# Optimization experiments

Hardware: AMD Instinct MI355X
Metric: run time of the kernel (lower is better)

The kernel has to match this reference:

```python
import jax, jax.numpy as jnp
import numpy as np
from jax import lax

EPS = 1e-5

def _bn(x, g, b, m, v):
    # eval-mode BatchNorm2d over channel dim of NCHW
    return (x - m[None, :, None, None]) * (g / jnp.sqrt(v + EPS))[None, :, None, None] + b[None, :, None, None]


def _forward(x, proj_w, proj_b, bn0_g, bn0_b, bn0_m, bn0_v,
             in_proj_w, conv_w, conv_b, x_proj_w, dt_w, dt_b, A_log, D,
             out_proj_w, fc_w, fc_b,
             c1_w, c1_b, bn1_g, bn1_b, bn1_m, bn1_v,
             c2_w, c2_b, bn2_g, bn2_b, bn2_m, bn2_v):
    d_state = A_log.shape[1]
    # ---- spectral projection: 1x1 conv + BN + ReLU ----
    p = jnp.einsum('bchw,dc->bdhw', x, proj_w) + proj_b[None, :, None, None]
    p = jax.nn.relu(_bn(p, bn0_g, bn0_b, bn0_m, bn0_v))
    b, d, h, w = p.shape
    L = h * w
    tok = p.reshape(b, d, L).transpose(0, 2, 1)            # [b, L, d_model]

    # ---- Mamba block (d_model=32, d_state=16, d_conv=4, expand=2) ----
    xz = tok @ in_proj_w.T                                 # [b, L, 2*d_in]
    d_in = xz.shape[-1] // 2
    xm, z = xz[..., :d_in], xz[..., d_in:]
    # causal depthwise conv1d along sequence
    xc = lax.conv_general_dilated(
        xm.transpose(0, 2, 1), conv_w[:, None, :], (1,),
        [(conv_w.shape[-1] - 1, 0)], feature_group_count=d_in,
        dimension_numbers=('NCH', 'OIH', 'NCH'))
    u = jax.nn.silu(xc + conv_b[None, :, None]).transpose(0, 2, 1)  # [b, L, d_in]
    xdbl = u @ x_proj_w.T                                  # [b, L, dt_rank+2N]
    dt_rank = dt_w.shape[1]
    dt = xdbl[..., :dt_rank]
    Bm = xdbl[..., dt_rank:dt_rank + d_state]              # [b, L, N]
    Cm = xdbl[..., dt_rank + d_state:]                     # [b, L, N]
    delta = jax.nn.softplus(dt @ dt_w.T + dt_b)            # [b, L, d_in]
    A = -jnp.exp(A_log)                                    # [d_in, N]

    def step(hst, inp):
        d_t, B_t, C_t, u_t = inp                           # [b,d_in],[b,N],[b,N],[b,d_in]
        dA = jnp.exp(d_t[..., None] * A)                   # [b, d_in, N]
        hst = dA * hst + (d_t * u_t)[..., None] * B_t[:, None, :]
        y_t = jnp.einsum('bdn,bn->bd', hst, C_t)
        return hst, y_t

    h0 = jnp.zeros((b, d_in, d_state), dtype=u.dtype)
    xs = (delta.transpose(1, 0, 2), Bm.transpose(1, 0, 2),
          Cm.transpose(1, 0, 2), u.transpose(1, 0, 2))
    _, ys = lax.scan(step, h0, xs)                         # [L, b, d_in]
    y = ys.transpose(1, 0, 2) + u * D                      # D skip
    y = y * jax.nn.silu(z)                                 # gated
    m_out = y @ out_proj_w.T                               # [b, L, d_model]
    mamba_feat = (m_out @ fc_w.T + fc_b).mean(axis=1)      # [b, FEATURE_DIM]

    # ---- CNN branch ----
    dn = ('NCHW', 'OIHW', 'NCHW')
    c = lax.conv_general_dilated(p, c1_w, (1, 1), 'VALID', dimension_numbers=dn) + c1_b[None, :, None, None]
    c = jax.nn.relu(_bn(c, bn1_g, bn1_b, bn1_m, bn1_v))
    c = lax.conv_general_dilated(c, c2_w, (1, 1), 'VALID', dimension_numbers=dn) + c2_b[None, :, None, None]
    c = jax.nn.relu(_bn(c, bn2_g, bn2_b, bn2_m, bn2_v))
    cnn_feat = c.mean(axis=(2, 3))                         # AdaptiveAvgPool2d(1)+Flatten
    return mamba_feat + cnn_feat


def setup_inputs() -> dict:
    key = jax.random.key(0)
    ks = jax.random.split(key, 16)
    B, C_IN, P = 128, 200, 32
    D_MODEL, D_IN, N, DTR, FDIM = 32, 64, 16, 2, 128
    r = lambda k, s, sc=0.05: jax.random.normal(k, s, jnp.float32) * sc
    f32 = jnp.float32
    return {
        'x': jax.random.normal(ks[0], (B, C_IN, P, P), f32),
        'proj_w': r(ks[1], (D_MODEL, C_IN)),
        'proj_b': jnp.zeros((D_MODEL,), f32),
        'bn0_g': jnp.ones((D_MODEL,), f32), 'bn0_b': jnp.zeros((D_MODEL,), f32),
        'bn0_m': jnp.zeros((D_MODEL,), f32), 'bn0_v': jnp.ones((D_MODEL,), f32),
        'in_proj_w': r(ks[2], (2 * D_IN, D_MODEL)),
        'conv_w': r(ks[3], (D_IN, 4), 0.3),
        'conv_b': jnp.zeros((D_IN,), f32),
        'x_proj_w': r(ks[4], (DTR + 2 * N, D_IN)),
        'dt_w': r(ks[5], (D_IN, DTR), 0.5),
        'dt_b': r(ks[6], (D_IN,), 0.5) - 4.0,
        'A_log': jnp.tile(jnp.log(jnp.arange(1, N + 1, dtype=f32))[None, :], (D_IN, 1)),
        'D': jnp.ones((D_IN,), f32),
        'out_proj_w': r(ks[7], (D_MODEL, D_IN)),
        'fc_w': r(ks[8], (FDIM, D_MODEL)),
        'fc_b': jnp.zeros((FDIM,), f32),
        'c1_w': r(ks[9], (32, D_MODEL, 3, 3)),
        'c1_b': jnp.zeros((32,), f32),
        'bn1_g': jnp.ones((32,), f32), 'bn1_b': jnp.zeros((32,), f32),
        'bn1_m': jnp.zeros((32,), f32), 'bn1_v': jnp.ones((32,), f32),
        'c2_w': r(ks[10], (FDIM, 32, 3, 3)),
        'c2_b': jnp.zeros((FDIM,), f32),
        'bn2_g': jnp.ones((FDIM,), f32), 'bn2_b': jnp.zeros((FDIM,), f32),
        'bn2_m': jnp.zeros((FDIM,), f32), 'bn2_v': jnp.ones((FDIM,), f32),
    }


def reference(x, proj_w, proj_b, bn0_g, bn0_b, bn0_m, bn0_v,
              in_proj_w, conv_w, conv_b, x_proj_w, dt_w, dt_b, A_log, D,
              out_proj_w, fc_w, fc_b,
              c1_w, c1_b, bn1_g, bn1_b, bn1_m, bn1_v,
              c2_w, c2_b, bn2_g, bn2_b, bn2_m, bn2_v):
    return _forward(x, proj_w, proj_b, bn0_g, bn0_b, bn0_m, bn0_v,
                    in_proj_w, conv_w, conv_b, x_proj_w, dt_w, dt_b, A_log, D,
                    out_proj_w, fc_w, fc_b,
                    c1_w, c1_b, bn1_g, bn1_b, bn1_m, bn1_v,
                    c2_w, c2_b, bn2_g, bn2_b, bn2_m, bn2_v)
```

## Files before the change

kernel.cpp:

```cpp
#include <hip/hip_runtime.h>
#include <cstdint>

typedef short bf16x8 __attribute__((ext_vector_type(8)));
typedef float f32x4 __attribute__((ext_vector_type(4)));
#define MFMA16(a, b, c) __builtin_amdgcn_mfma_f32_16x16x32_bf16((a), (b), (c), 0, 0, 0)

static __device__ __forceinline__ float fastrcp(float x) {
  float r;
  asm("v_rcp_f32 %0, %1" : "=v"(r) : "v"(x));
  return r;
}
static __device__ __forceinline__ float fastexp2(float x) {
  float r;
  asm("v_exp_f32 %0, %1" : "=v"(r) : "v"(x));
  return r;
}
static __device__ __forceinline__ float silu_(float x) {
  return x * fastrcp(1.f + __expf(-x));
}
static __device__ __forceinline__ unsigned short f2bf(float f) {
  union { float f; unsigned u; } v; v.f = f;
  unsigned r = v.u + 0x7FFF + ((v.u >> 16) & 1);
  return (unsigned short)(r >> 16);
}
static __device__ __forceinline__ void bf2x(unsigned p, float& lo, float& hi) {
  union { unsigned u; float f; } a, bb;
  a.u = p << 16; bb.u = p & 0xffff0000u;
  lo = a.f; hi = bb.f;
}
static __device__ __forceinline__ float bflo(unsigned short h) {
  union { unsigned u; float f; } a;
  a.u = ((unsigned)h) << 16;
  return a.f;
}

__global__ __launch_bounds__(256) void k_prep(
    const float* __restrict__ c1_w, const float* __restrict__ c2_w,
    const float* __restrict__ fc_w, const float* __restrict__ opw,
    const float* __restrict__ in_w, const float* __restrict__ xp_w,
    const float* __restrict__ pw,
    unsigned short* __restrict__ Wf1, unsigned short* __restrict__ Wf2,
    unsigned short* __restrict__ Wfin, unsigned short* __restrict__ Wfxp,
    unsigned short* __restrict__ Wfp,
    float* __restrict__ W2, float* __restrict__ cnn_sum)
{
  int i = blockIdx.x * 256 + threadIdx.x;
  if (i < 36864) {
    int j = i & 7, l = (i >> 3) & 63, m = (i >> 9) & 7, t = i >> 12;
    int co = m * 16 + (l & 15), ci = ((l >> 4) << 3) + j;
    Wf2[i] = f2bf(c2_w[(size_t)(co * 32 + ci) * 9 + t]);
  } else if (i < 46080) {
    int ii = i - 36864;
    int j = ii & 7, l = (ii >> 3) & 63, m = (ii >> 9) & 1, t = ii >> 10;
    int co = m * 16 + (l & 15), ci = ((l >> 4) << 3) + j;
    Wf1[ii] = f2bf(c1_w[(size_t)(co * 32 + ci) * 9 + t]);
  } else if (i < 54272) {
    int ii = i - 46080;
    int f = ii >> 6, d2 = ii & 63;
    float a = 0.f;
    #pragma unroll
    for (int dm = 0; dm < 32; dm++) a = fmaf(fc_w[(f << 5) + dm], opw[(dm << 6) + d2], a);
    W2[ii] = a;
  } else if (i < 70656) {
    cnn_sum[i - 54272] = 0.f;
  } else if (i < 74752) {
    int ii = i - 70656;
    int j = ii & 7, l = (ii >> 3) & 63, ot = ii >> 9;
    int o = (ot << 4) + (l & 15), c = ((l >> 4) << 3) + j;
    Wfin[ii] = f2bf(in_w[(o << 5) + c]);
  } else if (i < 77824) {
    int ii = i - 74752;
    int j = ii & 7, l = (ii >> 3) & 63, kh = (ii >> 9) & 1, ot = ii >> 10;
    int jr = (ot << 4) + (l & 15), c = (kh << 5) + ((l >> 4) << 3) + j;
    Wfxp[ii] = (jr < 34) ? f2bf(xp_w[(jr << 6) + c]) : (unsigned short)0;
  } else if (i < 84992) {
    int ii = i - 77824;
    int j = ii & 7, l = (ii >> 3) & 63, m = (ii >> 9) & 1, kt = ii >> 10;
    int co = (m << 4) + (l & 15), c = (kt << 5) + ((l >> 4) << 3) + j;
    Wfp[ii] = (c < 200) ? f2bf(pw[co * 200 + c]) : (unsigned short)0;
  }
}

__global__ __launch_bounds__(256, 4) void k_proj_m(
    const float* __restrict__ x, const unsigned short* __restrict__ Wfp,
    const float* __restrict__ pb,
    const float* __restrict__ g, const float* __restrict__ be,
    const float* __restrict__ mm, const float* __restrict__ vv,
    unsigned short* __restrict__ p_bf)
{
  __shared__ __align__(16) unsigned xT[2][256 * 20];
  int b = blockIdx.x >> 2, l0 = (blockIdx.x & 3) << 8;
  int tid = threadIdx.x, lane = tid & 63, w = tid >> 6;
  int li = lane & 15, kg4 = (lane >> 4) << 2;
  float scv[2][4], sbv[2][4];
  #pragma unroll
  for (int m = 0; m < 2; m++)
    #pragma unroll
    for (int jj = 0; jj < 4; jj++) {
      int co = m * 16 + ((lane >> 4) << 2) + jj;
      float s = g[co] * rsqrtf(vv[co] + 1e-5f);
      scv[m][jj] = s;
      sbv[m][jj] = fmaf(pb[co] - mm[co], s, be[co]);
    }
  const float* xb = x + (size_t)b * 200 * 1024 + l0 + tid;
  #pragma unroll
  for (int p = 0; p < 16; p++) {
    float v0 = xb[(2 * p) << 10];
    float v1 = xb[(2 * p + 1) << 10];
    xT[0][tid * 20 + p] = (unsigned)f2bf(v0) | ((unsigned)f2bf(v1) << 16);
  }
  __syncthreads();
  f32x4 acc[4][2];
  #pragma unroll
  for (int q = 0; q < 4; q++) {
    acc[q][0] = (f32x4){0.f, 0.f, 0.f, 0.f};
    acc[q][1] = (f32x4){0.f, 0.f, 0.f, 0.f};
  }
  int buf = 0;
  for (int kt = 0; kt < 7; kt++) {
    if (kt < 6) {
      const float* xc = xb + (((size_t)(kt + 1)) << 15);
      int cb = (kt + 1) * 32;
      #pragma unroll
      for (int p = 0; p < 16; p++) {
        int c = cb + 2 * p;
        float v0 = (c < 200) ? xc[(2 * p) << 10] : 0.f;
        float v1 = (c + 1 < 200) ? xc[(2 * p + 1) << 10] : 0.f;
        xT[buf ^ 1][tid * 20 + p] = (unsigned)f2bf(v0) | ((unsigned)f2bf(v1) << 16);
      }
    }
    bf16x8 a0 = *reinterpret_cast<const bf16x8*>(&Wfp[(((kt << 1) + 0) * 64 + lane) << 3]);
    bf16x8 a1 = *reinterpret_cast<const bf16x8*>(&Wfp[(((kt << 1) + 1) * 64 + lane) << 3]);
    #pragma unroll
    for (int q = 0; q < 4; q++) {
      int px = ((w + (q << 2)) << 4) + li;
      bf16x8 bfr = *reinterpret_cast<const bf16x8*>(&xT[buf][px * 20 + kg4]);
      acc[q][0] = MFMA16(a0, bfr, acc[q][0]);
      acc[q][1] = MFMA16(a1, bfr, acc[q][1]);
    }
    __syncthreads();
    buf ^= 1;
  }
  #pragma unroll
  for (int q = 0; q < 4; q++) {
    int px = ((w + (q << 2)) << 4) + li;
    size_t obase = (((size_t)b << 10) + l0 + px) << 5;
    #pragma unroll
    for (int m = 0; m < 2; m++) {
      f32x4 av = acc[q][m];
      ushort4 pk;
      pk.x = f2bf(fmaxf(fmaf(av[0], scv[m][0], sbv[m][0]), 0.f));
      pk.y = f2bf(fmaxf(fmaf(av[1], scv[m][1], sbv[m][1]), 0.f));
      pk.z = f2bf(fmaxf(fmaf(av[2], scv[m][2], sbv[m][2]), 0.f));
      pk.w = f2bf(fmaxf(fmaf(av[3], scv[m][3], sbv[m][3]), 0.f));
      *reinterpret_cast<ushort4*>(&p_bf[obase + m * 16 + ((lane >> 4) << 2)]) = pk;
    }
  }
}

__global__ __launch_bounds__(1024, 4) void k_mamba(
    const unsigned short* __restrict__ p_bf,
    const unsigned short* __restrict__ Wfin,
    const unsigned short* __restrict__ Wfxp,
    const float* __restrict__ conv_w,
    const float* __restrict__ conv_b,
    const float* __restrict__ dt_w,
    const float* __restrict__ dt_b,
    const float* __restrict__ A_log,
    float* __restrict__ pqrs,
    float* __restrict__ au_g)
{
  __shared__ __align__(16) char smem[65072];
  float* xm  = (float*)smem;
  float* dlS = (float*)smem;
  unsigned short* ubS  = (unsigned short*)(smem + 18224);
  unsigned short* uTb  = (unsigned short*)(smem + 27440);
  unsigned short* duzP = (unsigned short*)(smem + 36656);
  float* bcT  = (float*)(smem + 54064);
  float* cwS  = (float*)(smem + 62768);
  float* cbS  = (float*)(smem + 63792);
  float* dtwS = (float*)(smem + 64048);
  float* dtbS = (float*)(smem + 64560);
  float* auS  = (float*)(smem + 64816);

  int b = blockIdx.x >> 4, ch = blockIdx.x & 15;
  int tid = threadIdx.x, lane = tid & 63, w = tid >> 6;
  int li = lane & 15, cig8 = (lane >> 4) << 3;

  if (tid < 256) cwS[tid] = conv_w[tid];
  else if (tid < 320) cbS[tid - 256] = conv_b[tid - 256];
  else if (tid < 448) dtwS[tid - 320] = dt_w[tid - 320];
  else if (tid < 512) dtbS[tid - 448] = dt_b[tid - 448];
  else if (tid < 576) auS[tid - 512] = 0.f;

  const unsigned short* pbf_b = p_bf + ((size_t)b << 15);

  for (int j = w; j < 36; j += 16) {
    if (j < 20) {
      int ot = j / 5, tt = j % 5;
      int r = tt * 16 + li;
      int tg = (ch << 6) + r - 3;
      bf16x8 bfr = {0,0,0,0,0,0,0,0};
      if (r < 67 && tg >= 0)
        bfr = *reinterpret_cast<const bf16x8*>(pbf_b + ((size_t)tg << 5) + cig8);
      bf16x8 aW = *reinterpret_cast<const bf16x8*>(&Wfin[((ot << 6) + lane) << 3]);
      f32x4 acc = {0.f, 0.f, 0.f, 0.f};
      acc = MFMA16(aW, bfr, acc);
      if (r < 67)
        *reinterpret_cast<float4*>(&xm[r * 68 + (ot << 4) + ((lane >> 4) << 2)]) =
            make_float4(acc[0], acc[1], acc[2], acc[3]);
    } else {
      int jz = j - 20;
      int zot = jz >> 2, tt = jz & 3;
      int t = tt * 16 + li;
      int tg = (ch << 6) + t;
      bf16x8 bfr = *reinterpret_cast<const bf16x8*>(pbf_b + ((size_t)tg << 5) + cig8);
      bf16x8 aW = *reinterpret_cast<const bf16x8*>(&Wfin[(((4 + zot) << 6) + lane) << 3]);
      f32x4 acc = {0.f, 0.f, 0.f, 0.f};
      acc = MFMA16(aW, bfr, acc);
      int dzb = (zot << 4) + ((lane >> 4) << 2);
      int toff = ((t >> 2) << 3) + 4 + (t & 3);
      #pragma unroll
      for (int q = 0; q < 4; q++)
        duzP[(dzb + q) * 136 + toff] = f2bf(silu_(acc[q]));
    }
  }
  __syncthreads();
  {
    int d2 = tid & 63, oct = tid >> 6;
    int t0 = oct << 2;
    float4 cw4 = *reinterpret_cast<const float4*>(&cwS[d2 << 2]);
    float cb1 = cbS[d2];
    float x0 = xm[t0 * 68 + d2], x1 = xm[(t0 + 1) * 68 + d2], x2 = xm[(t0 + 2) * 68 + d2];
    uint2 zz2 = *reinterpret_cast<const uint2*>(&duzP[d2 * 136 + (oct << 3) + 4]);
    float zf[4];
    bf2x(zz2.x, zf[0], zf[1]); bf2x(zz2.y, zf[2], zf[3]);
    unsigned short up[4];
    float aup = 0.f;
    #pragma unroll
    for (int s = 0; s < 4; s++) {
      int t = t0 + s;
      float x3 = xm[(t + 3) * 68 + d2];
      float a = cb1;
      a = fmaf(cw4.x, x0, a); a = fmaf(cw4.y, x1, a);
      a = fmaf(cw4.z, x2, a); a = fmaf(cw4.w, x3, a);
      float uu = silu_(a);
      unsigned short ub_ = f2bf(uu);
      ubS[t * 72 + d2] = ub_;
      up[s] = ub_;
      aup = fmaf(uu, zf[s], aup);
      x0 = x1; x1 = x2; x2 = x3;
    }
    uint2 pk;
    pk.x = (unsigned)up[0] | ((unsigned)up[1] << 16);
    pk.y = (unsigned)up[2] | ((unsigned)up[3] << 16);
    *reinterpret_cast<uint2*>(&uTb[d2 * 72 + t0]) = pk;
    atomicAdd(&auS[d2], aup);
  }
  __syncthreads();
  if (w < 12) {
    int ot = w >> 2, tt = w & 3;
    int t = tt * 16 + li;
    const unsigned short* ub = &ubS[t * 72];
    bf16x8 b0 = *reinterpret_cast<const bf16x8*>(ub + cig8);
    bf16x8 b1 = *reinterpret_cast<const bf16x8*>(ub + 32 + cig8);
    bf16x8 a0 = *reinterpret_cast<const bf16x8*>(&Wfxp[(((ot << 1) + 0) * 64 + lane) << 3]);
    bf16x8 a1 = *reinterpret_cast<const bf16x8*>(&Wfxp[(((ot << 1) + 1) * 64 + lane) << 3]);
    f32x4 acc = {0.f, 0.f, 0.f, 0.f};
    acc = MFMA16(a0, b0, acc);
    acc = MFMA16(a1, b1, acc);
    int jb = (ot << 4) + ((lane >> 4) << 2);
    #pragma unroll
    for (int q = 0; q < 4; q++) {
      int jj = jb + q;
      if (jj < 2) bcT[(t & 31) * 68 + 64 + (jj << 1) + (t >> 5)] = acc[q];
      else if (jj < 34) bcT[(jj - 2) * 68 + t] = acc[q];
    }
  }
  __syncthreads();
  {
    int t = tid >> 4, dq = (tid & 15) << 2;
    int tr = t & 31, th = t >> 5;
    float d0 = bcT[tr * 68 + 64 + th];
    float d1 = bcT[tr * 68 + 66 + th];
    int toff = ((t >> 2) << 3) + (t & 3);
    #pragma unroll
    for (int q = 0; q < 4; q++) {
      int dg = dq + q;
      float pre = fmaf(d0, dtwS[dg << 1], fmaf(d1, dtwS[(dg << 1) + 1], dtbS[dg]));
      float dl_ = (pre > 20.f) ? pre : __logf(1.f + __expf(pre));
      dlS[dg * 68 + t] = dl_;
      float uf = bflo(uTb[dg * 72 + t]);
      duzP[dg * 136 + toff] = f2bf(dl_ * uf);
    }
  }
  __syncthreads();
  {
    int sd = tid >> 4, sn = tid & 15;
    float Areg2 = -__expf(A_log[(sd << 4) + sn]) * 1.44269504f;
    float P = 1.f, qq = 0.f, R = 0.f, S = 0.f;
    const float* dr = &dlS[sd * 68];
    const unsigned short* dz = &duzP[sd * 136];
    const float* Br = &bcT[sn * 68];
    const float* Cr = &bcT[(16 + sn) * 68];
    for (int g = 0; g < 16; g++) {
      float4 dv = *reinterpret_cast<const float4*>(dr + (g << 2));
      uint4 duz = *reinterpret_cast<const uint4*>(dz + (g << 3));
      float4 Bv = *reinterpret_cast<const float4*>(Br + (g << 2));
      float4 Cv = *reinterpret_cast<const float4*>(Cr + (g << 2));
      float du0, du1, du2, du3, z0, z1, z2, z3;
      bf2x(duz.x, du0, du1); bf2x(duz.y, du2, du3);
      bf2x(duz.z, z0, z1);  bf2x(duz.w, z2, z3);
      float e0 = fastexp2(dv.x * Areg2), e1 = fastexp2(dv.y * Areg2);
      float e2 = fastexp2(dv.z * Areg2), e3 = fastexp2(dv.w * Areg2);
      float c0 = Cv.x * z0, c1 = Cv.y * z1, c2 = Cv.z * z2, c3 = Cv.w * z3;
      P = e0 * P; qq = fmaf(e0, qq, du0 * Bv.x); R = fmaf(c0, P, R); S = fmaf(c0, qq, S);
      P = e1 * P; qq = fmaf(e1, qq, du1 * Bv.y); R = fmaf(c1, P, R); S = fmaf(c1, qq, S);
      P = e2 * P; qq = fmaf(e2, qq, du2 * Bv.z); R = fmaf(c2, P, R); S = fmaf(c2, qq, S);
      P = e3 * P; qq = fmaf(e3, qq, du3 * Bv.w); R = fmaf(c3, P, R); S = fmaf(c3, qq, S);
    }
    size_t idx = ((((size_t)b << 4) + ch) << 10) + (sd << 4) + sn;
    *reinterpret_cast<float4*>(pqrs + (idx << 2)) = make_float4(P, qq, R, S);
    if (sn == 0) au_g[((((size_t)b << 4) + ch) << 6) + sd] = auS[sd];
  }
}

__global__ __launch_bounds__(512) void k_comb(
    const float* __restrict__ pqrs, const float* __restrict__ au_g,
    const float* __restrict__ Dp, float* __restrict__ ybar)
{
  int b = blockIdx.x >> 1, hh = blockIdx.x & 1;
  int tid = threadIdx.x;
  int sd = (hh << 5) + (tid >> 4), sn = tid & 15;
  float4 pq[16];
  #pragma unroll
  for (int c = 0; c < 16; c++) {
    size_t idx = ((((size_t)b << 4) + c) << 10) + (sd << 4) + sn;
    pq[c] = *reinterpret_cast<const float4*>(pqrs + (idx << 2));
  }
  float h = 0.f, y = 0.f;
  #pragma unroll
  for (int c = 0; c < 16; c++) {
    y = fmaf(pq[c].z, h, y + pq[c].w);
    h = fmaf(pq[c].x, h, pq[c].y);
  }
  float val = y + Dp[sd] * au_g[((((size_t)b << 4) + sn) << 6) + sd];
  val += __shfl_xor(val, 1); val += __shfl_xor(val, 2);
  val += __shfl_xor(val, 4); val += __shfl_xor(val, 8);
  if (sn == 0) ybar[(b << 6) + sd] = val * (1.f / 1024.f);
}

__global__ __launch_bounds__(256) void k_conv1m(
    const unsigned short* __restrict__ p_bf, const unsigned short* __restrict__ Wf1,
    const float* __restrict__ cbias,
    const float* __restrict__ g, const float* __restrict__ be,
    const float* __restrict__ mm, const float* __restrict__ vv,
    unsigned short* __restrict__ c1_bf)
{
  __shared__ __align__(16) unsigned short inS[8 * 32 * 40];
  int b = blockIdx.x / 5, s = blockIdx.x % 5;
  int y0 = s * 6;
  int tid = threadIdx.x, lane = tid & 63, w = tid >> 6;
  int li = lane & 15, cig8 = (lane >> 4) << 3;
  for (int uu = tid; uu < 1024; uu += 256) {
    int r = uu >> 7, rem = uu & 127;
    uint4 v = *reinterpret_cast<const uint4*>(
        &p_bf[((((size_t)b << 10) + (y0 + r) * 32) << 5) + rem * 8]);
    int xx = rem >> 2, cg = rem & 3;
    *reinterpret_cast<uint4*>(&inS[(r * 32 + xx) * 40 + cg * 8]) = v;
  }
  bf16x8 aw[9][2];
  #pragma unroll
  for (int t = 0; t < 9; t++)
    #pragma unroll
    for (int m = 0; m < 2; m++)
      aw[t][m] = *reinterpret_cast<const bf16x8*>(&Wf1[(((t << 1) + m) * 64 + lane) * 8]);
  float scv[2][4], sbv[2][4];
  #pragma unroll
  for (int m = 0; m < 2; m++)
    #pragma unroll
    for (int j = 0; j < 4; j++) {
      int co = m * 16 + ((lane >> 4) << 2) + j;
      float sc = g[co] * rsqrtf(vv[co] + 1e-5f);
      scv[m][j] = sc;
      sbv[m][j] = fmaf(cbias[co] - mm[co], sc, be[co]);
    }
  __syncthreads();
  #pragma unroll
  for (int q = 0; q < 3; q++) {
    int pf = w + q * 4;
    int p = pf * 16 + li;
    int pv = (p < 180) ? p : 0;
    int ry = pv / 30, rx = pv % 30;
    f32x4 a0 = {0.f, 0.f, 0.f, 0.f}, a1 = {0.f, 0.f, 0.f, 0.f};
    #pragma unroll
    for (int t = 0; t < 9; t++) {
      int dy = t / 3, dx = t % 3;
      bf16x8 bfr = *reinterpret_cast<const bf16x8*>(
          &inS[((ry + dy) * 32 + rx + dx) * 40 + cig8]);
      a0 = MFMA16(aw[t][0], bfr, a0);
      a1 = MFMA16(aw[t][1], bfr, a1);
    }
    if (p < 180) {
      size_t obase = ((size_t)b * 900 + (size_t)(y0 + ry) * 30 + rx) << 5;
      #pragma unroll
      for (int m = 0; m < 2; m++) {
        f32x4 av = m ? a1 : a0;
        ushort4 pk;
        pk.x = f2bf(fmaxf(fmaf(av[0], scv[m][0], sbv[m][0]), 0.f));
        pk.y = f2bf(fmaxf(fmaf(av[1], scv[m][1], sbv[m][1]), 0.f));
        pk.z = f2bf(fmaxf(fmaf(av[2], scv[m][2], sbv[m][2]), 0.f));
        pk.w = f2bf(fmaxf(fmaf(av[3], scv[m][3], sbv[m][3]), 0.f));
        *reinterpret_cast<ushort4*>(&c1_bf[obase + m * 16 + ((lane >> 4) << 2)]) = pk;
      }
    }
  }
}

__global__ __launch_bounds__(256) void k_conv2m(
    const unsigned short* __restrict__ c1_bf, const unsigned short* __restrict__ Wf2,
    const float* __restrict__ cb2,
    const float* __restrict__ g, const float* __restrict__ be,
    const float* __restrict__ mm, const float* __restrict__ vv,
    float* __restrict__ cnn_sum)
{
  __shared__ __align__(16) unsigned short inS[6 * 30 * 40];
  int b = blockIdx.x / 7, s = blockIdx.x % 7;
  int y0 = s * 4;
  int tid = threadIdx.x, lane = tid & 63, w = tid >> 6;
  int li = lane & 15, cig8 = (lane >> 4) << 3;
  for (int uu = tid; uu < 720; uu += 256) {
    int r = uu / 120, rem = uu % 120;
    uint4 v = *reinterpret_cast<const uint4*>(
        &c1_bf[(((size_t)b * 900 + (size_t)(y0 + r) * 30) << 5) + rem * 8]);
    int xx = rem >> 2, cg = rem & 3;
    *reinterpret_cast<uint4*>(&inS[(r * 30 + xx) * 40 + cg * 8]) = v;
  }
  bf16x8 aw[9][2];
  #pragma unroll
  for (int t = 0; t < 9; t++)
    #pragma unroll
    for (int m = 0; m < 2; m++)
      aw[t][m] = *reinterpret_cast<const bf16x8*>(&Wf2[(((t << 3) + (w << 1) + m) * 64 + lane) * 8]);
  float scv[2][4], sbv[2][4];
  float psum[2][4] = {{0.f,0.f,0.f,0.f},{0.f,0.f,0.f,0.f}};
  #pragma unroll
  for (int m = 0; m < 2; m++)
    #pragma unroll
    for (int j = 0; j < 4; j++) {
      int co = (w << 5) + m * 16 + ((lane >> 4) << 2) + j;
      float sc = g[co] * rsqrtf(vv[co] + 1e-5f);
      scv[m][j] = sc;
      sbv[m][j] = fmaf(cb2[co] - mm[co], sc, be[co]);
    }
  __syncthreads();
  #pragma unroll
  for (int pf = 0; pf < 7; pf++) {
    int p = pf * 16 + li;
    int ry = p / 28, rx = p % 28;
    f32x4 a0 = {0.f, 0.f, 0.f, 0.f}, a1 = {0.f, 0.f, 0.f, 0.f};
    #pragma unroll
    for (int t = 0; t < 9; t++) {
      int dy = t / 3, dx = t % 3;
      bf16x8 bfr = *reinterpret_cast<const bf16x8*>(
          &inS[((ry + dy) * 30 + rx + dx) * 40 + cig8]);
      a0 = MFMA16(aw[t][0], bfr, a0);
      a1 = MFMA16(aw[t][1], bfr, a1);
    }
    #pragma unroll
    for (int j = 0; j < 4; j++) {
      psum[0][j] += fmaxf(fmaf(a0[j], scv[0][j], sbv[0][j]), 0.f);
      psum[1][j] += fmaxf(fmaf(a1[j], scv[1][j], sbv[1][j]), 0.f);
    }
  }
  #pragma unroll
  for (int m = 0; m < 2; m++)
    #pragma unroll
    for (int j = 0; j < 4; j++) {
      float v = psum[m][j];
      v += __shfl_xor(v, 1); v += __shfl_xor(v, 2);
      v += __shfl_xor(v, 4); v += __shfl_xor(v, 8);
      if (li == 0) {
        int co = (w << 5) + m * 16 + ((lane >> 4) << 2) + j;
        atomicAdd(&cnn_sum[((size_t)b << 7) + co], v);
      }
    }
}

__global__ __launch_bounds__(256) void k_final(
    const float* __restrict__ ybar, const float* __restrict__ W2,
    const float* __restrict__ fc_b, const float* __restrict__ cnn_sum,
    float* __restrict__ out)
{
  int i = blockIdx.x * 256 + threadIdx.x;
  int b = i >> 7, f = i & 127;
  float a = 0.f;
  #pragma unroll
  for (int d2 = 0; d2 < 64; d2++) a = fmaf(ybar[(b << 6) + d2], W2[(f << 6) + d2], a);
  out[i] = a + fc_b[f] + cnn_sum[i] * (1.f / 784.f);
}

extern "C" void kernel_launch(void* const* d_in, const int* in_sizes, int n_in,
                              void* d_out, int out_size, void* d_ws, size_t ws_size,
                              hipStream_t stream) {
  (void)in_sizes; (void)n_in; (void)out_size; (void)ws_size;
  const float* x         = (const float*)d_in[0];
  const float* proj_w    = (const float*)d_in[1];
  const float* proj_b    = (const float*)d_in[2];
  const float* bn0_g     = (const float*)d_in[3];
  const float* bn0_b     = (const float*)d_in[4];
  const float* bn0_m     = (const float*)d_in[5];
  const float* bn0_v     = (const float*)d_in[6];
  const float* in_proj_w = (const float*)d_in[7];
  const float* conv_w    = (const float*)d_in[8];
  const float* conv_b    = (const float*)d_in[9];
  const float* x_proj_w  = (const float*)d_in[10];
  const float* dt_w      = (const float*)d_in[11];
  const float* dt_b      = (const float*)d_in[12];
  const float* A_log     = (const float*)d_in[13];
  const float* Dp        = (const float*)d_in[14];
  const float* out_proj_w= (const float*)d_in[15];
  const float* fc_w      = (const float*)d_in[16];
  const float* fc_b      = (const float*)d_in[17];
  const float* c1_w      = (const float*)d_in[18];
  const float* c1_b      = (const float*)d_in[19];
  const float* bn1_g     = (const float*)d_in[20];
  const float* bn1_b     = (const float*)d_in[21];
  const float* bn1_m     = (const float*)d_in[22];
  const float* bn1_v     = (const float*)d_in[23];
  const float* c2_w      = (const float*)d_in[24];
  const float* c2_b      = (const float*)d_in[25];
  const float* bn2_g     = (const float*)d_in[26];
  const float* bn2_b     = (const float*)d_in[27];
  const float* bn2_m     = (const float*)d_in[28];
  const float* bn2_v     = (const float*)d_in[29];
  float* out = (float*)d_out;
  float* ws  = (float*)d_ws;
  float* ybar    = ws;
  float* cnn_sum = ws + 8192;
  float* W2      = ws + 24576;
  float* pqrs    = ws + 32768;
  float* au_g    = ws + 8421376;
  unsigned short* p_bf  = (unsigned short*)(ws + 8552448);
  unsigned short* c1_bf = (unsigned short*)(ws + 10649600);
  unsigned short* Wf1   = (unsigned short*)(ws + 12492800);
  unsigned short* Wf2   = (unsigned short*)(ws + 12497408);
  unsigned short* Wfin  = (unsigned short*)(ws + 12515840);
  unsigned short* Wfxp  = (unsigned short*)(ws + 12517888);
  unsigned short* Wfp   = (unsigned short*)(ws + 12519424);

  k_prep<<<dim3(332), dim3(256), 0, stream>>>(c1_w, c2_w, fc_w, out_proj_w, in_proj_w, x_proj_w,
                                              proj_w, Wf1, Wf2, Wfin, Wfxp, Wfp, W2, cnn_sum);
  k_proj_m<<<dim3(512), dim3(256), 0, stream>>>(x, Wfp, proj_b, bn0_g, bn0_b, bn0_m, bn0_v, p_bf);
  k_mamba<<<dim3(2048), dim3(1024), 0, stream>>>(p_bf, Wfin, Wfxp, conv_w, conv_b, dt_w, dt_b,
                                                 A_log, pqrs, au_g);
  k_comb<<<dim3(256), dim3(512), 0, stream>>>(pqrs, au_g, Dp, ybar);
  k_conv1m<<<dim3(640), dim3(256), 0, stream>>>(p_bf, Wf1, c1_b, bn1_g, bn1_b, bn1_m, bn1_v, c1_bf);
  k_conv2m<<<dim3(896), dim3(256), 0, stream>>>(c1_bf, Wf2, c2_b, bn2_g, bn2_b, bn2_m, bn2_v, cnn_sum);
  k_final<<<dim3(64), dim3(256), 0, stream>>>(ybar, W2, fc_b, cnn_sum, out);
}
```

Baseline: 135.1 us.

## Merge weight prep into projection kernel and fold scan-combine into conv2 launch

Merges the weight-prep kernel with the spectral projection kernel: each projection block now converts its own copy of the projection weights into shared memory, and extra blocks do the remaining weight prep. The chunk-combine kernel becomes extra blocks of the conv2 kernel, which drops two kernel launches and their serialization gaps. The scan loop also prefetches the next group's LDS operands one iteration ahead. In exchange, every projection block redoes the projection weight conversion, the larger shared-memory footprint (55 KB) may lower occupancy, and the prefetch adds registers.

```diff
diff --git a/kernel.cpp b/kernel.cpp
--- a/kernel.cpp
+++ b/kernel.cpp
@@ -34,80 +34,80 @@
   return a.f;
 }
 
-__global__ __launch_bounds__(256) void k_prep(
+__global__ __launch_bounds__(256, 4) void k_front(
+    const float* __restrict__ x, const float* __restrict__ pw,
+    const float* __restrict__ pb,
+    const float* __restrict__ g0, const float* __restrict__ be0,
+    const float* __restrict__ mm0, const float* __restrict__ vv0,
     const float* __restrict__ c1_w, const float* __restrict__ c2_w,
     const float* __restrict__ fc_w, const float* __restrict__ opw,
     const float* __restrict__ in_w, const float* __restrict__ xp_w,
-    const float* __restrict__ pw,
+    unsigned short* __restrict__ p_bf,
     unsigned short* __restrict__ Wf1, unsigned short* __restrict__ Wf2,
     unsigned short* __restrict__ Wfin, unsigned short* __restrict__ Wfxp,
-    unsigned short* __restrict__ Wfp,
     float* __restrict__ W2, float* __restrict__ cnn_sum)
 {
-  int i = blockIdx.x * 256 + threadIdx.x;
-  if (i < 36864) {
-    int j = i & 7, l = (i >> 3) & 63, m = (i >> 9) & 7, t = i >> 12;
-    int co = m * 16 + (l & 15), ci = ((l >> 4) << 3) + j;
-    Wf2[i] = f2bf(c2_w[(size_t)(co * 32 + ci) * 9 + t]);
-  } else if (i < 46080) {
-    int ii = i - 36864;
-    int j = ii & 7, l = (ii >> 3) & 63, m = (ii >> 9) & 1, t = ii >> 10;
-    int co = m * 16 + (l & 15), ci = ((l >> 4) << 3) + j;
-    Wf1[ii] = f2bf(c1_w[(size_t)(co * 32 + ci) * 9 + t]);
-  } else if (i < 54272) {
-    int ii = i - 46080;
-    int f = ii >> 6, d2 = ii & 63;
-    float a = 0.f;
-    #pragma unroll
-    for (int dm = 0; dm < 32; dm++) a = fmaf(fc_w[(f << 5) + dm], opw[(dm << 6) + d2], a);
-    W2[ii] = a;
-  } else if (i < 70656) {
-    cnn_sum[i - 54272] = 0.f;
-  } else if (i < 74752) {
-    int ii = i - 70656;
-    int j = ii & 7, l = (ii >> 3) & 63, ot = ii >> 9;
-    int o = (ot << 4) + (l & 15), c = ((l >> 4) << 3) + j;
-    Wfin[ii] = f2bf(in_w[(o << 5) + c]);
-  } else if (i < 77824) {
-    int ii = i - 74752;
-    int j = ii & 7, l = (ii >> 3) & 63, kh = (ii >> 9) & 1, ot = ii >> 10;
-    int jr = (ot << 4) + (l & 15), c = (kh << 5) + ((l >> 4) << 3) + j;
-    Wfxp[ii] = (jr < 34) ? f2bf(xp_w[(jr << 6) + c]) : (unsigned short)0;
-  } else if (i < 84992) {
-    int ii = i - 77824;
-    int j = ii & 7, l = (ii >> 3) & 63, m = (ii >> 9) & 1, kt = ii >> 10;
+  __shared__ __align__(16) char fsm[55296];
+  int tid = threadIdx.x;
+  if (blockIdx.x >= 512) {
+    int i = (blockIdx.x - 512) * 256 + tid;
+    if (i < 36864) {
+      int j = i & 7, l = (i >> 3) & 63, m = (i >> 9) & 7, t = i >> 12;
+      int co = m * 16 + (l & 15), ci = ((l >> 4) << 3) + j;
+      Wf2[i] = f2bf(c2_w[(size_t)(co * 32 + ci) * 9 + t]);
+    } else if (i < 46080) {
+      int ii = i - 36864;
+      int j = ii & 7, l = (ii >> 3) & 63, m = (ii >> 9) & 1, t = ii >> 10;
+      int co = m * 16 + (l & 15), ci = ((l >> 4) << 3) + j;
+      Wf1[ii] = f2bf(c1_w[(size_t)(co * 32 + ci) * 9 + t]);
+    } else if (i < 54272) {
+      int ii = i - 46080;
+      int f = ii >> 6, d2 = ii & 63;
+      float a = 0.f;
+      #pragma unroll
+      for (int dm = 0; dm < 32; dm++) a = fmaf(fc_w[(f << 5) + dm], opw[(dm << 6) + d2], a);
+      W2[ii] = a;
+    } else if (i < 70656) {
+      cnn_sum[i - 54272] = 0.f;
+    } else if (i < 74752) {
+      int ii = i - 70656;
+      int j = ii & 7, l = (ii >> 3) & 63, ot = ii >> 9;
+      int o = (ot << 4) + (l & 15), c = ((l >> 4) << 3) + j;
+      Wfin[ii] = f2bf(in_w[(o << 5) + c]);
+    } else if (i < 77824) {
+      int ii = i - 74752;
+      int j = ii & 7, l = (ii >> 3) & 63, kh = (ii >> 9) & 1, ot = ii >> 10;
+      int jr = (ot << 4) + (l & 15), c = (kh << 5) + ((l >> 4) << 3) + j;
+      Wfxp[ii] = (jr < 34) ? f2bf(xp_w[(jr << 6) + c]) : (unsigned short)0;
+    }
+    return;
+  }
+  unsigned* xT = (unsigned*)fsm;
+  unsigned short* WfpL = (unsigned short*)(fsm + 40960);
+  int b = blockIdx.x >> 2, l0 = (blockIdx.x & 3) << 8;
+  int lane = tid & 63, w = tid >> 6;
+  int li = lane & 15, kg4 = (lane >> 4) << 2;
+  for (int i = tid; i < 7168; i += 256) {
+    int j = i & 7, l = (i >> 3) & 63, m = (i >> 9) & 1, kt = i >> 10;
     int co = (m << 4) + (l & 15), c = (kt << 5) + ((l >> 4) << 3) + j;
-    Wfp[ii] = (c < 200) ? f2bf(pw[co * 200 + c]) : (unsigned short)0;
-  }
-}
-
-__global__ __launch_bounds__(256, 4) void k_proj_m(
-    const float* __restrict__ x, const unsigned short* __restrict__ Wfp,
-    const float* __restrict__ pb,
-    const float* __restrict__ g, const float* __restrict__ be,
-    const float* __restrict__ mm, const float* __restrict__ vv,
-    unsigned short* __restrict__ p_bf)
-{
-  __shared__ __align__(16) unsigned xT[2][256 * 20];
-  int b = blockIdx.x >> 2, l0 = (blockIdx.x & 3) << 8;
-  int tid = threadIdx.x, lane = tid & 63, w = tid >> 6;
-  int li = lane & 15, kg4 = (lane >> 4) << 2;
+    WfpL[i] = (c < 200) ? f2bf(pw[co * 200 + c]) : (unsigned short)0;
+  }
   float scv[2][4], sbv[2][4];
   #pragma unroll
   for (int m = 0; m < 2; m++)
     #pragma unroll
     for (int jj = 0; jj < 4; jj++) {
       int co = m * 16 + ((lane >> 4) << 2) + jj;
-      float s = g[co] * rsqrtf(vv[co] + 1e-5f);
+      float s = g0[co] * rsqrtf(vv0[co] + 1e-5f);
       scv[m][jj] = s;
-      sbv[m][jj] = fmaf(pb[co] - mm[co], s, be[co]);
+      sbv[m][jj] = fmaf(pb[co] - mm0[co], s, be0[co]);
     }
   const float* xb = x + (size_t)b * 200 * 1024 + l0 + tid;
   #pragma unroll
   for (int p = 0; p < 16; p++) {
     float v0 = xb[(2 * p) << 10];
     float v1 = xb[(2 * p + 1) << 10];
-    xT[0][tid * 20 + p] = (unsigned)f2bf(v0) | ((unsigned)f2bf(v1) << 16);
+    xT[tid * 20 + p] = (unsigned)f2bf(v0) | ((unsigned)f2bf(v1) << 16);
   }
   __syncthreads();
   f32x4 acc[4][2];
@@ -126,15 +126,15 @@
         int c = cb + 2 * p;
         float v0 = (c < 200) ? xc[(2 * p) << 10] : 0.f;
         float v1 = (c + 1 < 200) ? xc[(2 * p + 1) << 10] : 0.f;
-        xT[buf ^ 1][tid * 20 + p] = (unsigned)f2bf(v0) | ((unsigned)f2bf(v1) << 16);
+        xT[(buf ^ 1) * 5120 + tid * 20 + p] = (unsigned)f2bf(v0) | ((unsigned)f2bf(v1) << 16);
       }
     }
-    bf16x8 a0 = *reinterpret_cast<const bf16x8*>(&Wfp[(((kt << 1) + 0) * 64 + lane) << 3]);
-    bf16x8 a1 = *reinterpret_cast<const bf16x8*>(&Wfp[(((kt << 1) + 1) * 64 + lane) << 3]);
+    bf16x8 a0 = *reinterpret_cast<const bf16x8*>(&WfpL[(((kt << 1) + 0) * 64 + lane) << 3]);
+    bf16x8 a1 = *reinterpret_cast<const bf16x8*>(&WfpL[(((kt << 1) + 1) * 64 + lane) << 3]);
     #pragma unroll
     for (int q = 0; q < 4; q++) {
       int px = ((w + (q << 2)) << 4) + li;
-      bf16x8 bfr = *reinterpret_cast<const bf16x8*>(&xT[buf][px * 20 + kg4]);
+      bf16x8 bfr = *reinterpret_cast<const bf16x8*>(&xT[buf * 5120 + px * 20 + kg4]);
       acc[q][0] = MFMA16(a0, bfr, acc[q][0]);
       acc[q][1] = MFMA16(a1, bfr, acc[q][1]);
     }
@@ -303,51 +303,33 @@
     const unsigned short* dz = &duzP[sd * 136];
     const float* Br = &bcT[sn * 68];
     const float* Cr = &bcT[(16 + sn) * 68];
+    float4 dv = *reinterpret_cast<const float4*>(dr);
+    uint4 duz = *reinterpret_cast<const uint4*>(dz);
+    float4 Bv = *reinterpret_cast<const float4*>(Br);
+    float4 Cv = *reinterpret_cast<const float4*>(Cr);
     for (int g = 0; g < 16; g++) {
-      float4 dv = *reinterpret_cast<const float4*>(dr + (g << 2));
-      uint4 duz = *reinterpret_cast<const uint4*>(dz + (g << 3));
-      float4 Bv = *reinterpret_cast<const float4*>(Br + (g << 2));
-      float4 Cv = *reinterpret_cast<const float4*>(Cr + (g << 2));
+      float4 dvc = dv; uint4 dzc = duz; float4 Bvc = Bv; float4 Cvc = Cv;
+      if (g < 15) {
+        dv  = *reinterpret_cast<const float4*>(dr + ((g + 1) << 2));
+        duz = *reinterpret_cast<const uint4*>(dz + ((g + 1) << 3));
+        Bv  = *reinterpret_cast<const float4*>(Br + ((g + 1) << 2));
+        Cv  = *reinterpret_cast<const float4*>(Cr + ((g + 1) << 2));
+      }
       float du0, du1, du2, du3, z0, z1, z2, z3;
-      bf2x(duz.x, du0, du1); bf2x(duz.y, du2, du3);
-      bf2x(duz.z, z0, z1);  bf2x(duz.w, z2, z3);
-      float e0 = fastexp2(dv.x * Areg2), e1 = fastexp2(dv.y * Areg2);
-      float e2 = fastexp2(dv.z * Areg2), e3 = fastexp2(dv.w * Areg2);
-      float c0 = Cv.x * z0, c1 = Cv.y * z1, c2 = Cv.z * z2, c3 = Cv.w * z3;
-      P = e0 * P; qq = fmaf(e0, qq, du0 * Bv.x); R = fmaf(c0, P, R); S = fmaf(c0, qq, S);
-      P = e1 * P; qq = fmaf(e1, qq, du1 * Bv.y); R = fmaf(c1, P, R); S = fmaf(c1, qq, S);
-      P = e2 * P; qq = fmaf(e2, qq, du2 * Bv.z); R = fmaf(c2, P, R); S = fmaf(c2, qq, S);
-      P = e3 * P; qq = fmaf(e3, qq, du3 * Bv.w); R = fmaf(c3, P, R); S = fmaf(c3, qq, S);
+      bf2x(dzc.x, du0, du1); bf2x(dzc.y, du2, du3);
+      bf2x(dzc.z, z0, z1);  bf2x(dzc.w, z2, z3);
+      float e0 = fastexp2(dvc.x * Areg2), e1 = fastexp2(dvc.y * Areg2);
+      float e2 = fastexp2(dvc.z * Areg2), e3 = fastexp2(dvc.w * Areg2);
+      float c0 = Cvc.x * z0, c1 = Cvc.y * z1, c2 = Cvc.z * z2, c3 = Cvc.w * z3;
+      P = e0 * P; qq = fmaf(e0, qq, du0 * Bvc.x); R = fmaf(c0, P, R); S = fmaf(c0, qq, S);
+      P = e1 * P; qq = fmaf(e1, qq, du1 * Bvc.y); R = fmaf(c1, P, R); S = fmaf(c1, qq, S);
+      P = e2 * P; qq = fmaf(e2, qq, du2 * Bvc.z); R = fmaf(c2, P, R); S = fmaf(c2, qq, S);
+      P = e3 * P; qq = fmaf(e3, qq, du3 * Bvc.w); R = fmaf(c3, P, R); S = fmaf(c3, qq, S);
     }
     size_t idx = ((((size_t)b << 4) + ch) << 10) + (sd << 4) + sn;
     *reinterpret_cast<float4*>(pqrs + (idx << 2)) = make_float4(P, qq, R, S);
     if (sn == 0) au_g[((((size_t)b << 4) + ch) << 6) + sd] = auS[sd];
   }
-}
-
-__global__ __launch_bounds__(512) void k_comb(
-    const float* __restrict__ pqrs, const float* __restrict__ au_g,
-    const float* __restrict__ Dp, float* __restrict__ ybar)
-{
-  int b = blockIdx.x >> 1, hh = blockIdx.x & 1;
-  int tid = threadIdx.x;
-  int sd = (hh << 5) + (tid >> 4), sn = tid & 15;
-  float4 pq[16];
-  #pragma unroll
-  for (int c = 0; c < 16; c++) {
-    size_t idx = ((((size_t)b << 4) + c) << 10) + (sd << 4) + sn;
-    pq[c] = *reinterpret_cast<const float4*>(pqrs + (idx << 2));
-  }
-  float h = 0.f, y = 0.f;
-  #pragma unroll
-  for (int c = 0; c < 16; c++) {
-    y = fmaf(pq[c].z, h, y + pq[c].w);
-    h = fmaf(pq[c].x, h, pq[c].y);
-  }
-  float val = y + Dp[sd] * au_g[((((size_t)b << 4) + sn) << 6) + sd];
-  val += __shfl_xor(val, 1); val += __shfl_xor(val, 2);
-  val += __shfl_xor(val, 4); val += __shfl_xor(val, 8);
-  if (sn == 0) ybar[(b << 6) + sd] = val * (1.f / 1024.f);
 }
 
 __global__ __launch_bounds__(256) void k_conv1m(
@@ -417,17 +399,42 @@
   }
 }
 
-__global__ __launch_bounds__(256) void k_conv2m(
+__global__ __launch_bounds__(256) void k_back(
     const unsigned short* __restrict__ c1_bf, const unsigned short* __restrict__ Wf2,
     const float* __restrict__ cb2,
     const float* __restrict__ g, const float* __restrict__ be,
     const float* __restrict__ mm, const float* __restrict__ vv,
-    float* __restrict__ cnn_sum)
+    const float* __restrict__ pqrs, const float* __restrict__ au_g,
+    const float* __restrict__ Dp,
+    float* __restrict__ cnn_sum, float* __restrict__ ybar)
 {
   __shared__ __align__(16) unsigned short inS[6 * 30 * 40];
+  int tid = threadIdx.x;
+  if (blockIdx.x >= 896) {
+    int cb = blockIdx.x - 896;
+    int b = cb >> 2, qq4 = cb & 3;
+    int sd = (qq4 << 4) + (tid >> 4), sn = tid & 15;
+    float4 pq[16];
+    #pragma unroll
+    for (int c = 0; c < 16; c++) {
+      size_t idx = ((((size_t)b << 4) + c) << 10) + (sd << 4) + sn;
+      pq[c] = *reinterpret_cast<const float4*>(pqrs + (idx << 2));
+    }
+    float h = 0.f, y = 0.f;
+    #pragma unroll
+    for (int c = 0; c < 16; c++) {
+      y = fmaf(pq[c].z, h, y + pq[c].w);
+      h = fmaf(pq[c].x, h, pq[c].y);
+    }
+    float val = y + Dp[sd] * au_g[((((size_t)b << 4) + sn) << 6) + sd];
+    val += __shfl_xor(val, 1); val += __shfl_xor(val, 2);
+    val += __shfl_xor(val, 4); val += __shfl_xor(val, 8);
+    if (sn == 0) ybar[(b << 6) + sd] = val * (1.f / 1024.f);
+    return;
+  }
   int b = blockIdx.x / 7, s = blockIdx.x % 7;
   int y0 = s * 4;
-  int tid = threadIdx.x, lane = tid & 63, w = tid >> 6;
+  int lane = tid & 63, w = tid >> 6;
   int li = lane & 15, cig8 = (lane >> 4) << 3;
   for (int uu = tid; uu < 720; uu += 256) {
     int r = uu / 120, rem = uu % 120;
@@ -547,15 +554,14 @@
   unsigned short* Wf2   = (unsigned short*)(ws + 12497408);
   unsigned short* Wfin  = (unsigned short*)(ws + 12515840);
   unsigned short* Wfxp  = (unsigned short*)(ws + 12517888);
-  unsigned short* Wfp   = (unsigned short*)(ws + 12519424);
-
-  k_prep<<<dim3(332), dim3(256), 0, stream>>>(c1_w, c2_w, fc_w, out_proj_w, in_proj_w, x_proj_w,
-                                              proj_w, Wf1, Wf2, Wfin, Wfxp, Wfp, W2, cnn_sum);
-  k_proj_m<<<dim3(512), dim3(256), 0, stream>>>(x, Wfp, proj_b, bn0_g, bn0_b, bn0_m, bn0_v, p_bf);
+
+  k_front<<<dim3(816), dim3(256), 0, stream>>>(x, proj_w, proj_b, bn0_g, bn0_b, bn0_m, bn0_v,
+                                               c1_w, c2_w, fc_w, out_proj_w, in_proj_w, x_proj_w,
+                                               p_bf, Wf1, Wf2, Wfin, Wfxp, W2, cnn_sum);
   k_mamba<<<dim3(2048), dim3(1024), 0, stream>>>(p_bf, Wfin, Wfxp, conv_w, conv_b, dt_w, dt_b,
                                                  A_log, pqrs, au_g);
-  k_comb<<<dim3(256), dim3(512), 0, stream>>>(pqrs, au_g, Dp, ybar);
   k_conv1m<<<dim3(640), dim3(256), 0, stream>>>(p_bf, Wf1, c1_b, bn1_g, bn1_b, bn1_m, bn1_v, c1_bf);
-  k_conv2m<<<dim3(896), dim3(256), 0, stream>>>(c1_bf, Wf2, c2_b, bn2_g, bn2_b, bn2_m, bn2_v, cnn_sum);
+  k_back<<<dim3(1408), dim3(256), 0, stream>>>(c1_bf, Wf2, c2_b, bn2_g, bn2_b, bn2_m, bn2_v,
+                                               pqrs, au_g, Dp, cnn_sum, ybar);
   k_final<<<dim3(64), dim3(256), 0, stream>>>(ybar, W2, fc_b, cnn_sum, out);
 }
```

Result: faster. 129.8 us (-3.9%).
